# Kernel optimization log

Hardware: AMD Instinct MI355X
Metric: run time of the kernel (lower is better)

## Reference

```python
import jax, jax.numpy as jnp
import numpy as np

B, CIN, HALF, H, W = 4, 3, 32, 512, 512
K_MODE, PAD_MODE, N_LEVELS = 11, 5, 17  # 11x11 mode window, reflect pad 5, round(x*255/16) in 0..16
SLOPE, EPS = 0.01, 1e-5


def _leaky(x):
    return jnp.where(x > 0, x, SLOPE * x)


def _bn(x, g, b):
    # BatchNorm2d in training mode: batch statistics over (B,H,W), biased var
    m = x.mean(axis=(0, 2, 3), keepdims=True)
    v = x.var(axis=(0, 2, 3), keepdims=True)
    return (x - m) * jax.lax.rsqrt(v + EPS) * g[None, :, None, None] + b[None, :, None, None]


def _mode_pool(x):
    # quantize to 17 discrete levels, then sliding-window histogram mode (fused
    # equivalent of unfold + torch.mode; argmax first-hit == smallest tied value)
    k = jnp.clip(jnp.round(x * (255.0 / 16.0)), 0, N_LEVELS - 1).astype(jnp.int32)
    kp = jnp.pad(k, ((0, 0), (0, 0), (PAD_MODE, PAD_MODE), (PAD_MODE, PAD_MODE)), mode='reflect')
    onehot = (kp[..., None] == jnp.arange(N_LEVELS, dtype=jnp.int32)).astype(jnp.float32)
    counts = jax.lax.reduce_window(onehot, 0.0, jax.lax.add,
                                   (1, 1, K_MODE, K_MODE, 1), (1, 1, 1, 1, 1), 'VALID')
    mode_k = jnp.argmax(counts, axis=-1)  # [B,C,H,W]
    return mode_k.astype(jnp.float32) * (16.0 / 256.0)


def _nearest(x, Ho, Wo):
    # torch interpolate(mode='nearest'): src = floor(dst * in/out)
    hi, wi = x.shape[2], x.shape[3]
    ri = (jnp.arange(Ho) * hi) // Ho
    ci = (jnp.arange(Wo) * wi) // Wo
    return x[:, :, ri][:, :, :, ci]


def _forward(x, w1, b1, w2, b2, bn1_g, bn1_b, w3, b3, bn2_g, bn2_b,
             k_down, k_w, bnw_g, bnw_b, k_h, bnh_g, bnh_b):
    xm = _mode_pool(x)  # [B,CIN,H,W]
    # prepare: 1x1 conv -> LeakyReLU -> 1x1 conv -> BN -> LeakyReLU -> depthwise 1x1 -> BN -> LeakyReLU
    h = _leaky(jnp.einsum('bchw,oc->bohw', xm, w1) + b1[None, :, None, None])
    h = jnp.einsum('bchw,oc->bohw', h, w2) + b2[None, :, None, None]
    h = _leaky(_bn(h, bn1_g, bn1_b))
    h = h * w3[None, :, None, None] + b3[None, :, None, None]  # groups=half 1x1 conv
    h = _leaky(_bn(h, bn2_g, bn2_b))
    Bs, half, Ho, Wo = h.shape
    score = jnp.zeros((Bs, 2 * half, Ho, Wo), jnp.float32)
    d = h
    while min(d.shape[2], d.shape[3]) >= 3:  # static pyramid: 512->171->57->19->7->3->1
        d = jax.lax.conv_general_dilated(d, k_down, (3, 3), ((1, 1), (1, 1)),
                                         dimension_numbers=('NCHW', 'OIHW', 'NCHW'),
                                         feature_group_count=half)
        z = _nearest(d, Ho, Wo)
        wbr = _leaky(_bn(z * k_w[None, :, None, None], bnw_g, bnw_b))  # width branch (SharedConv k=1, no bias)
        hbr = _leaky(_bn(z * k_h[None, :, None, None], bnh_g, bnh_b))  # height branch
        # stack(dim=1).reshape => width channels first, then height channels
        score = score + jnp.concatenate([wbr, hbr], axis=1)
    return score


def setup_inputs():
    key = jax.random.key(0)
    ks = jax.random.split(key, 8)
    x = jax.random.uniform(ks[0], (B, CIN, H, W), dtype=jnp.float32)
    s1, s2 = 1.0 / np.sqrt(CIN), 1.0 / np.sqrt(2 * CIN)
    return {
        'x': x,
        'w1': jax.random.uniform(ks[1], (2 * CIN, CIN), jnp.float32, -s1, s1),
        'b1': jax.random.uniform(ks[2], (2 * CIN,), jnp.float32, -s1, s1),
        'w2': jax.random.uniform(ks[3], (HALF, 2 * CIN), jnp.float32, -s2, s2),
        'b2': jax.random.uniform(ks[4], (HALF,), jnp.float32, -s2, s2),
        'bn1_g': jnp.ones((HALF,), jnp.float32),
        'bn1_b': jnp.zeros((HALF,), jnp.float32),
        'w3': jax.random.uniform(ks[5], (HALF,), jnp.float32, -1.0, 1.0),
        'b3': jax.random.uniform(ks[6], (HALF,), jnp.float32, -1.0, 1.0),
        'bn2_g': jnp.ones((HALF,), jnp.float32),
        'bn2_b': jnp.zeros((HALF,), jnp.float32),
        'k_down': jnp.full((HALF, 1, 3, 3), 0.5, jnp.float32),  # SharedConv init
        'k_w': jnp.full((HALF,), 0.5, jnp.float32),
        'bnw_g': jnp.ones((HALF,), jnp.float32),
        'bnw_b': jnp.zeros((HALF,), jnp.float32),
        'k_h': jnp.full((HALF,), 0.5, jnp.float32),
        'bnh_g': jnp.ones((HALF,), jnp.float32),
        'bnh_b': jnp.zeros((HALF,), jnp.float32),
    }


def reference(x, w1, b1, w2, b2, bn1_g, bn1_b, w3, b3, bn2_g, bn2_b,
              k_down, k_w, bnw_g, bnw_b, k_h, bnh_g, bnh_b):
    return _forward(x, w1, b1, w2, b2, bn1_g, bn1_b, w3, b3, bn2_g, bn2_b,
                    k_down, k_w, bnw_g, bnw_b, k_h, bnh_g, bnh_b)
```

## Files before the change

### kernel.cpp

```cpp
#include <hip/hip_runtime.h>

#define HH 512
#define WW 512
#define HW 262144
#define NPIX 1048576
#define NPIXF 1048576.0f

typedef float f4 __attribute__((ext_vector_type(4)));

__device__ __forceinline__ float leaky(float v) { return v > 0.f ? v : 0.01f * v; }

__device__ __forceinline__ float repw(int i, int s) {
    return (float)(((i + 1) * 512 + s - 1) / s - (i * 512 + s - 1) / s);
}

__device__ __forceinline__ void hins(unsigned long long& h0, unsigned long long& h1,
                                     unsigned& c16, int val) {
    unsigned long long inc = 1ull << ((val & 7) * 8);
    h0 += (val < 8) ? inc : 0;
    h1 += (val >= 8 && val < 16) ? inc : 0;
    c16 += (unsigned)(val >> 4);
}
__device__ __forceinline__ void hrem(unsigned long long& h0, unsigned long long& h1,
                                     unsigned& c16, int val) {
    unsigned long long inc = 1ull << ((val & 7) * 8);
    h0 -= (val < 8) ? inc : 0;
    h1 -= (val >= 8 && val < 16) ? inc : 0;
    c16 -= (unsigned)(val >> 4);
}

__global__ __launch_bounds__(256) void mode_kernel(const float* __restrict__ x,
                                                   unsigned char* __restrict__ modeq) {
    __shared__ unsigned char q[26 * 272];
    __shared__ unsigned ch[2][267 * 5];
    const int plane = blockIdx.z;
    const int tc0 = blockIdx.x * 256;
    const int tr0 = blockIdx.y * 16;
    const float* xp = x + (size_t)plane * HW;
    for (int idx = threadIdx.x; idx < 26 * 266; idx += 256) {
        int r = idx / 266;
        int cc = idx - r * 266;
        int gr = tr0 + r - 5; gr = gr < 0 ? -gr : (gr > 511 ? 1022 - gr : gr);
        int gc = tc0 + cc - 5; gc = gc < 0 ? -gc : (gc > 511 ? 1022 - gc : gc);
        float v = rintf(xp[gr * WW + gc] * 15.9375f);
        v = fminf(fmaxf(v, 0.f), 16.f);
        q[r * 272 + cc] = (unsigned char)(int)v;
    }
    const int t = threadIdx.x;
    unsigned long long A0 = 0, A1 = 0; unsigned A2 = 0;
    unsigned long long B0 = 0, B1 = 0; unsigned B2 = 0;
    __syncthreads();
    for (int r = 0; r < 16; ++r) {
        if (r == 0) {
            #pragma unroll
            for (int v = 0; v < 11; ++v) {
                hins(A0, A1, A2, q[v * 272 + t]);
                if (t < 10) hins(B0, B1, B2, q[v * 272 + 256 + t]);
            }
        } else {
            hrem(A0, A1, A2, q[(r - 1) * 272 + t]);
            hins(A0, A1, A2, q[(r + 10) * 272 + t]);
            if (t < 10) {
                hrem(B0, B1, B2, q[(r - 1) * 272 + 256 + t]);
                hins(B0, B1, B2, q[(r + 10) * 272 + 256 + t]);
            }
        }
        unsigned* cb = ch[r & 1];
        cb[t * 5 + 0] = (unsigned)A0;
        cb[t * 5 + 1] = (unsigned)(A0 >> 32);
        cb[t * 5 + 2] = (unsigned)A1;
        cb[t * 5 + 3] = (unsigned)(A1 >> 32);
        cb[t * 5 + 4] = A2;
        if (t < 10) {
            cb[(256 + t) * 5 + 0] = (unsigned)B0;
            cb[(256 + t) * 5 + 1] = (unsigned)(B0 >> 32);
            cb[(256 + t) * 5 + 2] = (unsigned)B1;
            cb[(256 + t) * 5 + 3] = (unsigned)(B1 >> 32);
            cb[(256 + t) * 5 + 4] = B2;
        }
        __syncthreads();
        unsigned long long H0 = 0, H1 = 0; unsigned C = 0;
        #pragma unroll
        for (int v = 0; v < 11; ++v) {
            const unsigned* p = &cb[(t + v) * 5];
            H0 += (unsigned long long)p[0] | ((unsigned long long)p[1] << 32);
            H1 += (unsigned long long)p[2] | ((unsigned long long)p[3] << 32);
            C += p[4];
        }
        unsigned m = 0;
        #pragma unroll
        for (int i = 0; i < 8; ++i) {
            unsigned cnt = (unsigned)(H0 >> (8 * i)) & 0xFFu;
            unsigned val = (cnt << 8) | (unsigned)(16 - i);
            m = m > val ? m : val;
        }
        #pragma unroll
        for (int i = 8; i < 16; ++i) {
            unsigned cnt = (unsigned)(H1 >> (8 * (i - 8))) & 0xFFu;
            unsigned val = (cnt << 8) | (unsigned)(16 - i);
            m = m > val ? m : val;
        }
        unsigned val16 = (C << 8);
        m = m > val16 ? m : val16;
        int k = 16 - (int)(m & 0xFFu);
        modeq[(size_t)plane * HW + (size_t)(tr0 + r) * WW + tc0 + t] = (unsigned char)k;
    }
}

__global__ __launch_bounds__(256) void hist_kernel(const unsigned char* __restrict__ modeq,
                                                   const float* __restrict__ w1,
                                                   const float* __restrict__ b1,
                                                   unsigned* __restrict__ partial,
                                                   float* __restrict__ mpart) {
    __shared__ unsigned lh[4913];
    __shared__ float mred[27][4];
    for (int i = threadIdx.x; i < 4913; i += 256) lh[i] = 0;
    __syncthreads();
    int base = blockIdx.x * 8192;
    int b = base >> 18;
    int hw0 = base & (HW - 1);
    const unsigned char* mp = modeq + (size_t)b * 3 * HW;
    #pragma unroll
    for (int j = 0; j < 8; ++j) {
        int g = threadIdx.x + 256 * j;
        int hw = hw0 + g * 4;
        unsigned u0 = *(const unsigned*)(mp + hw);
        unsigned u1 = *(const unsigned*)(mp + hw + HW);
        unsigned u2 = *(const unsigned*)(mp + hw + 2 * HW);
        #pragma unroll
        for (int k = 0; k < 4; ++k) {
            int k0 = (u0 >> (8 * k)) & 0xFF;
            int k1 = (u1 >> (8 * k)) & 0xFF;
            int k2 = (u2 >> (8 * k)) & 0xFF;
            atomicAdd(&lh[k0 + 17 * k1 + 289 * k2], 1u);
        }
    }
    __syncthreads();
    unsigned* pp = partial + blockIdx.x * 4913;
    for (int i = threadIdx.x; i < 4913; i += 256) pp[i] = lh[i];
    float w1r[18], b1r[6];
    #pragma unroll
    for (int k = 0; k < 18; ++k) w1r[k] = w1[k];
    #pragma unroll
    for (int o = 0; o < 6; ++o) b1r[o] = b1[o];
    float M[27];
    #pragma unroll
    for (int i = 0; i < 27; ++i) M[i] = 0.f;
    for (int bin = threadIdx.x; bin < 4913; bin += 256) {
        float cnt = (float)lh[bin];
        int k0 = bin % 17;
        int r = bin / 17;
        int k1 = r % 17;
        int k2 = r / 17;
        float xm0 = k0 * 0.0625f, xm1 = k1 * 0.0625f, xm2 = k2 * 0.0625f;
        float t1[6];
        #pragma unroll
        for (int o = 0; o < 6; ++o)
            t1[o] = leaky(xm0 * w1r[o * 3] + xm1 * w1r[o * 3 + 1] + xm2 * w1r[o * 3 + 2] + b1r[o]);
        #pragma unroll
        for (int o = 0; o < 6; ++o) M[o] += cnt * t1[o];
        int ii = 6;
        #pragma unroll
        for (int j = 0; j < 6; ++j)
            #pragma unroll
            for (int k = j; k < 6; ++k) { M[ii] += cnt * t1[j] * t1[k]; ++ii; }
    }
    int wv = threadIdx.x >> 6;
    #pragma unroll
    for (int i = 0; i < 27; ++i) {
        float v = M[i];
        #pragma unroll
        for (int off = 32; off >= 1; off >>= 1) v += __shfl_xor(v, off);
        if ((threadIdx.x & 63) == 0) mred[i][wv] = v;
    }
    __syncthreads();
    if (threadIdx.x < 27)
        mpart[blockIdx.x * 27 + threadIdx.x] =
            mred[threadIdx.x][0] + mred[threadIdx.x][1] +
            mred[threadIdx.x][2] + mred[threadIdx.x][3];
}

__global__ __launch_bounds__(256) void redA_kernel(const unsigned* __restrict__ partial,
                                                   float* __restrict__ histf,
                                                   const float* __restrict__ mpart,
                                                   const float* __restrict__ w2,
                                                   const float* __restrict__ b2,
                                                   const float* __restrict__ g1,
                                                   const float* __restrict__ bb1,
                                                   float* __restrict__ p1) {
    if (blockIdx.x < 20) {
        int bin = blockIdx.x * 256 + threadIdx.x;
        if (bin >= 4913) return;
        unsigned s = 0;
        for (int blk = 0; blk < 128; ++blk) s += partial[blk * 4913 + bin];
        histf[bin] = (float)s;
        return;
    }
    __shared__ float mom[27];
    int t = threadIdx.x;
    if (t < 27) {
        float s = 0.f;
        for (int blk = 0; blk < 128; ++blk) s += mpart[blk * 27 + t];
        mom[t] = s;
    }
    __syncthreads();
    if (t < 32) {
        float w2r[6];
        #pragma unroll
        for (int k = 0; k < 6; ++k) w2r[k] = w2[t * 6 + k];
        float b2c = b2[t];
        float wm1 = 0.f;
        #pragma unroll
        for (int k = 0; k < 6; ++k) wm1 += w2r[k] * mom[k];
        float q = 0.f;
        int ii = 6;
        #pragma unroll
        for (int j = 0; j < 6; ++j)
            #pragma unroll
            for (int k = j; k < 6; ++k) {
                float f = w2r[j] * w2r[k] * mom[ii];
                q += (j == k) ? f : 2.f * f;
                ++ii;
            }
        float mean = b2c + wm1 / NPIXF;
        float ex2 = b2c * b2c + 2.f * b2c * (wm1 / NPIXF) + q / NPIXF;
        float var = ex2 - mean * mean;
        float a = g1[t] * rsqrtf(var + 1e-5f);
        p1[t] = a;
        p1[32 + t] = bb1[t] - mean * a;
    }
}

__global__ __launch_bounds__(256) void solveB2_kernel(const float* __restrict__ histf,
                                                      const float* __restrict__ w1,
                                                      const float* __restrict__ b1,
                                                      const float* __restrict__ w2,
                                                      const float* __restrict__ b2,
                                                      const float* __restrict__ p1,
                                                      const float* __restrict__ w3,
                                                      const float* __restrict__ b3,
                                                      const float* __restrict__ g,
                                                      const float* __restrict__ bb,
                                                      float* __restrict__ p2) {
    __shared__ float rs[4], rq[4];
    int c = blockIdx.x;
    float w1r[18], b1r[6], w2r[6];
    #pragma unroll
    for (int k = 0; k < 18; ++k) w1r[k] = w1[k];
    #pragma unroll
    for (int o = 0; o < 6; ++o) b1r[o] = b1[o];
    #pragma unroll
    for (int k = 0; k < 6; ++k) w2r[k] = w2[c * 6 + k];
    float b2c = b2[c];
    float a1 = p1[c], c1 = p1[32 + c];
    float sm = 0.f, sq = 0.f;
    for (int bin = threadIdx.x; bin < 4913; bin += 256) {
        float cnt = histf[bin];
        int k0 = bin % 17;
        int r = bin / 17;
        int k1 = r % 17;
        int k2 = r / 17;
        float xm0 = k0 * 0.0625f, xm1 = k1 * 0.0625f, xm2 = k2 * 0.0625f;
        float t1[6];
        #pragma unroll
        for (int o = 0; o < 6; ++o)
            t1[o] = leaky(xm0 * w1r[o * 3] + xm1 * w1r[o * 3 + 1] + xm2 * w1r[o * 3 + 2] + b1r[o]);
        float h2 = b2c;
        #pragma unroll
        for (int k = 0; k < 6; ++k) h2 += w2r[k] * t1[k];
        float tt = leaky(a1 * h2 + c1);
        sm += cnt * tt;
        sq += cnt * tt * tt;
    }
    #pragma unroll
    for (int off = 32; off >= 1; off >>= 1) {
        sm += __shfl_xor(sm, off);
        sq += __shfl_xor(sq, off);
    }
    if ((threadIdx.x & 63) == 0) { rs[threadIdx.x >> 6] = sm; rq[threadIdx.x >> 6] = sq; }
    __syncthreads();
    if (threadIdx.x == 0) {
        float s = rs[0] + rs[1] + rs[2] + rs[3];
        float qq = rq[0] + rq[1] + rq[2] + rq[3];
        float mt = s / NPIXF;
        float vt = qq / NPIXF - mt * mt;
        float m2 = w3[c] * mt + b3[c];
        float v2 = w3[c] * w3[c] * vt;
        float a = g[c] * rsqrtf(v2 + 1e-5f);
        p2[c] = a;
        p2[32 + c] = bb[c] - m2 * a;
    }
}

__global__ __launch_bounds__(64) void d1_kernel(const unsigned char* __restrict__ modeq,
                                                const float* __restrict__ w1,
                                                const float* __restrict__ b1,
                                                const float* __restrict__ w2,
                                                const float* __restrict__ b2,
                                                const float* __restrict__ w3,
                                                const float* __restrict__ b3,
                                                const float* __restrict__ p1,
                                                const float* __restrict__ p2,
                                                const float* __restrict__ kd,
                                                float* __restrict__ d1) {
    int j = blockIdx.x * 64 + threadIdx.x;
    if (j >= 171) return;
    int i = blockIdx.y;
    int b = blockIdx.z;
    float acc[32];
    #pragma unroll
    for (int c = 0; c < 32; ++c) acc[c] = 0.f;
    const unsigned char* mp = modeq + (size_t)b * 3 * HW;
    #pragma unroll
    for (int u = 0; u < 3; ++u) {
        int r = 3 * i - 1 + u;
        if (r < 0 || r > 511) continue;
        #pragma unroll
        for (int v = 0; v < 3; ++v) {
            int col = 3 * j - 1 + v;
            if (col < 0 || col > 511) continue;
            int off = r * WW + col;
            float xm0 = mp[off] * 0.0625f, xm1 = mp[off + HW] * 0.0625f, xm2 = mp[off + 2 * HW] * 0.0625f;
            float t1[6];
            #pragma unroll
            for (int o = 0; o < 6; ++o)
                t1[o] = leaky(xm0 * w1[o * 3] + xm1 * w1[o * 3 + 1] + xm2 * w1[o * 3 + 2] + b1[o]);
            #pragma unroll
            for (int c = 0; c < 32; ++c) {
                float h2 = b2[c];
                #pragma unroll
                for (int k = 0; k < 6; ++k) h2 += w2[c * 6 + k] * t1[k];
                float t = leaky(h2 * p1[c] + p1[32 + c]);
                float uu = t * w3[c] + b3[c];
                float hv = leaky(uu * p2[c] + p2[32 + c]);
                acc[c] += hv * kd[c * 9 + u * 3 + v];
            }
        }
    }
    size_t base = ((size_t)(b * 32) * 171 + i) * 171 + j;
    #pragma unroll
    for (int c = 0; c < 32; ++c) d1[base + (size_t)c * 29241] = acc[c];
}

__device__ __forceinline__ void red_store(float sm, float sq, float* rsc, float* ps) {
    #pragma unroll
    for (int off = 32; off >= 1; off >>= 1) {
        sm += __shfl_xor(sm, off);
        sq += __shfl_xor(sq, off);
    }
    __syncthreads();
    int wv = threadIdx.x >> 6;
    if ((threadIdx.x & 63) == 0) { rsc[wv] = sm; rsc[8 + wv] = sq; }
    __syncthreads();
    if (threadIdx.x == 0) {
        ps[0] = rsc[0] + rsc[1] + rsc[2] + rsc[3];
        ps[1] = rsc[8] + rsc[9] + rsc[10] + rsc[11];
    }
}

__device__ __forceinline__ void lvl(const float* src, int sin, float* dstL,
                                    float* dstG, int sout, const float* kreg,
                                    float* rsc, float* ps) {
    float sm = 0.f, sq = 0.f;
    int n = sout * sout;
    for (int i = threadIdx.x; i < n; i += 256) {
        int oi = i / sout, oj = i - oi * sout;
        float acc = 0.f;
        #pragma unroll
        for (int u = 0; u < 3; ++u) {
            int r = 3 * oi - 1 + u;
            if ((unsigned)r >= (unsigned)sin) continue;
            #pragma unroll
            for (int v = 0; v < 3; ++v) {
                int cc = 3 * oj - 1 + v;
                if ((unsigned)cc >= (unsigned)sin) continue;
                acc += src[r * sin + cc] * kreg[u * 3 + v];
            }
        }
        dstG[i] = acc;
        if (dstL) dstL[i] = acc;
        float w = repw(oi, sout) * repw(oj, sout);
        sm += w * acc;
        sq += w * acc * acc;
    }
    red_store(sm, sq, rsc, ps);
}

__global__ __launch_bounds__(256) void pyramid_kernel(const float* __restrict__ d1,
                                                      float* __restrict__ d2,
                                                      float* __restrict__ d3,
                                                      float* __restrict__ d4,
                                                      float* __restrict__ d5,
                                                      float* __restrict__ d6,
                                                      const float* __restrict__ kd,
                                                      float* __restrict__ pstats) {
    __shared__ float buf2[3249];
    __shared__ float buf3[361];
    __shared__ float buf4[49];
    __shared__ float buf5[9];
    __shared__ float rsc[16];
    int bc = blockIdx.x;
    int c = bc & 31;
    float kreg[9];
    #pragma unroll
    for (int qq = 0; qq < 9; ++qq) kreg[qq] = kd[c * 9 + qq];
    float* ps = pstats + (size_t)bc * 12;
    const float* s1 = d1 + (size_t)bc * 29241;
    float sm = 0.f, sq = 0.f;
    for (int i = threadIdx.x; i < 29241; i += 256) {
        int oi = i / 171, oj = i - oi * 171;
        float w = repw(oi, 171) * repw(oj, 171);
        float v = s1[i];
        sm += w * v;
        sq += w * v * v;
    }
    red_store(sm, sq, rsc, ps + 0);
    lvl(s1, 171, buf2, d2 + (size_t)bc * 3249, 57, kreg, rsc, ps + 2);
    lvl(buf2, 57, buf3, d3 + (size_t)bc * 361, 19, kreg, rsc, ps + 4);
    lvl(buf3, 19, buf4, d4 + (size_t)bc * 49, 7, kreg, rsc, ps + 6);
    lvl(buf4, 7, buf5, d5 + (size_t)bc * 9, 3, kreg, rsc, ps + 8);
    lvl(buf5, 3, nullptr, d6 + bc, 1, kreg, rsc, ps + 10);
}

__global__ void fin3_kernel(const float* __restrict__ pstats, const float* __restrict__ kw,
                            const float* __restrict__ gw, const float* __restrict__ bw,
                            const float* __restrict__ kh, const float* __restrict__ gh,
                            const float* __restrict__ bh, float* __restrict__ lp) {
    int t = threadIdx.x;
    if (t >= 192) return;
    int l = t >> 5, c = t & 31;
    float sm = 0.f, sq = 0.f;
    #pragma unroll
    for (int b = 0; b < 4; ++b) {
        const float* ps = pstats + (size_t)(b * 32 + c) * 12 + 2 * l;
        sm += ps[0];
        sq += ps[1];
    }
    float mz = sm / NPIXF;
    float vz = sq / NPIXF - mz * mz;
    float kwc = kw[c];
    float aw = gw[c] * rsqrtf(kwc * kwc * vz + 1e-5f);
    float khc = kh[c];
    float ah = gh[c] * rsqrtf(khc * khc * vz + 1e-5f);
    float* o = lp + (size_t)(l * 32 + c) * 4;
    o[0] = kwc * aw;
    o[1] = bw[c] - kwc * mz * aw;
    o[2] = khc * ah;
    o[3] = bh[c] - khc * mz * ah;
}

__global__ __launch_bounds__(256) void final_kernel(const float* __restrict__ d1,
                                                    const float* __restrict__ d2,
                                                    const float* __restrict__ d3,
                                                    const float* __restrict__ d4,
                                                    const float* __restrict__ d5,
                                                    const float* __restrict__ d6,
                                                    const float* __restrict__ lp,
                                                    float* __restrict__ out) {
    const float* ds[6] = {d1, d2, d3, d4, d5, d6};
    const int ss[6] = {171, 57, 19, 7, 3, 1};
    int idx = blockIdx.x * 256 + threadIdx.x;
    #pragma unroll 1
    for (int it = 0; it < 16; ++it, idx += 524288) {
        int w4 = (idx & 127) << 2;
        int h = (idx >> 7) & 511;
        int c = (idx >> 16) & 31;
        int b = idx >> 21;
        float accw[4] = {0.f, 0.f, 0.f, 0.f};
        float acch[4] = {0.f, 0.f, 0.f, 0.f};
        #pragma unroll
        for (int l = 0; l < 6; ++l) {
            int s = ss[l];
            int sh = (h * s) >> 9;
            const float* base = ds[l] + ((size_t)(b * 32 + c) * s + sh) * s;
            const float* a = lp + (size_t)(l * 32 + c) * 4;
            float a0 = a[0], a1 = a[1], a2 = a[2], a3 = a[3];
            #pragma unroll
            for (int k = 0; k < 4; ++k) {
                int sw = ((w4 + k) * s) >> 9;
                float val = base[sw];
                accw[k] += leaky(val * a0 + a1);
                acch[k] += leaky(val * a2 + a3);
            }
        }
        size_t o = (((size_t)(b * 64 + c)) << 18) + ((size_t)h << 9) + w4;
        f4 vw = {accw[0], accw[1], accw[2], accw[3]};
        f4 vh = {acch[0], acch[1], acch[2], acch[3]};
        __builtin_nontemporal_store(vw, (f4*)(out + o));
        __builtin_nontemporal_store(vh, (f4*)(out + o + (((size_t)32) << 18)));
    }
}

extern "C" void kernel_launch(void* const* d_in, const int* in_sizes, int n_in,
                              void* d_out, int out_size, void* d_ws, size_t ws_size,
                              hipStream_t stream) {
    const float* x     = (const float*)d_in[0];
    const float* w1    = (const float*)d_in[1];
    const float* b1    = (const float*)d_in[2];
    const float* w2    = (const float*)d_in[3];
    const float* b2    = (const float*)d_in[4];
    const float* bn1g  = (const float*)d_in[5];
    const float* bn1b  = (const float*)d_in[6];
    const float* w3    = (const float*)d_in[7];
    const float* b3    = (const float*)d_in[8];
    const float* bn2g  = (const float*)d_in[9];
    const float* bn2b  = (const float*)d_in[10];
    const float* kd    = (const float*)d_in[11];
    const float* kw    = (const float*)d_in[12];
    const float* bnwg  = (const float*)d_in[13];
    const float* bnwb  = (const float*)d_in[14];
    const float* kh    = (const float*)d_in[15];
    const float* bnhg  = (const float*)d_in[16];
    const float* bnhb  = (const float*)d_in[17];
    float* out = (float*)d_out;

    char* ws = (char*)d_ws;
    unsigned char* modeq = (unsigned char*)ws;
    float* mpart  = (float*)(ws + 3145728);
    float* tpart  = (float*)(ws + 3145728 + 13824);
    float* pstats = (float*)(ws + 3145728 + 13824 + 8192);
    float* p1 = (float*)(ws + 3174400);
    float* p2 = p1 + 64;
    float* lp = p2 + 64;
    float* histf = (float*)(ws + 3178496);
    unsigned* partial = (unsigned*)(ws + 3178496 + 20480);
    float* d1 = (float*)(ws + 3198976 + 2515456);
    float* d2 = d1 + 3742848;
    float* d3 = d2 + 415872;
    float* d4 = d3 + 46208;
    float* d5 = d4 + 6272;
    float* d6 = d5 + 1152;
    (void)tpart;

    mode_kernel<<<dim3(2, 32, 12), 256, 0, stream>>>(x, modeq);
    hist_kernel<<<128, 256, 0, stream>>>(modeq, w1, b1, partial, mpart);
    redA_kernel<<<21, 256, 0, stream>>>(partial, histf, mpart, w2, b2, bn1g, bn1b, p1);
    solveB2_kernel<<<32, 256, 0, stream>>>(histf, w1, b1, w2, b2, p1,
                                           w3, b3, bn2g, bn2b, p2);
    d1_kernel<<<dim3(3, 171, 4), 64, 0, stream>>>(modeq, w1, b1, w2, b2, w3, b3,
                                                  p1, p2, kd, d1);
    pyramid_kernel<<<128, 256, 0, stream>>>(d1, d2, d3, d4, d5, d6, kd, pstats);
    fin3_kernel<<<1, 192, 0, stream>>>(pstats, kw, bnwg, bnwb, kh, bnhg, bnhb, lp);
    final_kernel<<<2048, 256, 0, stream>>>(d1, d2, d3, d4, d5, d6, lp, out);
}
```

Baseline: 468.3 us.

## Drop shared column-histogram exchange in mode kernel; double hist kernel blocks

The mode kernel no longer keeps per-column histograms and combines 11 of them through shared memory with a barrier every output row. Each thread now holds a full 11x11 window histogram and slides it down by removing and adding whole 11-byte rows, read from shared memory as three 32-bit words. This removes the per-row syncthreads and the 5-word shared-memory traffic, but each thread does 22 histogram updates per row instead of 2. Separately, the histogram kernel launches 256 blocks over half as many pixels each, which doubles the partial buffers and the reduction loop length.

```diff
diff --git a/kernel.cpp b/kernel.cpp
--- a/kernel.cpp
+++ b/kernel.cpp
@@ -29,10 +29,48 @@
     c16 -= (unsigned)(val >> 4);
 }
 
+__device__ __forceinline__ void win3(const unsigned char* q, int rr, int t,
+                                     unsigned& w0, unsigned& w1, unsigned& w2) {
+    const unsigned* p = (const unsigned*)(q + rr * 272 + (t & ~3));
+    unsigned a0 = p[0], a1 = p[1], a2 = p[2], a3 = p[3];
+    int sh = (t & 3) * 8;
+    unsigned long long u01 = ((unsigned long long)a1 << 32) | a0;
+    unsigned long long u12 = ((unsigned long long)a2 << 32) | a1;
+    unsigned long long u23 = ((unsigned long long)a3 << 32) | a2;
+    w0 = (unsigned)(u01 >> sh);
+    w1 = (unsigned)(u12 >> sh);
+    w2 = (unsigned)(u23 >> sh);
+}
+
+__device__ __forceinline__ void winadd(const unsigned char* q, int rr, int t,
+                                       unsigned long long& H0, unsigned long long& H1,
+                                       unsigned& C) {
+    unsigned w0, w1, w2;
+    win3(q, rr, t, w0, w1, w2);
+    #pragma unroll
+    for (int i = 0; i < 4; ++i) hins(H0, H1, C, (w0 >> (8 * i)) & 0xFF);
+    #pragma unroll
+    for (int i = 0; i < 4; ++i) hins(H0, H1, C, (w1 >> (8 * i)) & 0xFF);
+    #pragma unroll
+    for (int i = 0; i < 3; ++i) hins(H0, H1, C, (w2 >> (8 * i)) & 0xFF);
+}
+
+__device__ __forceinline__ void winrem(const unsigned char* q, int rr, int t,
+                                       unsigned long long& H0, unsigned long long& H1,
+                                       unsigned& C) {
+    unsigned w0, w1, w2;
+    win3(q, rr, t, w0, w1, w2);
+    #pragma unroll
+    for (int i = 0; i < 4; ++i) hrem(H0, H1, C, (w0 >> (8 * i)) & 0xFF);
+    #pragma unroll
+    for (int i = 0; i < 4; ++i) hrem(H0, H1, C, (w1 >> (8 * i)) & 0xFF);
+    #pragma unroll
+    for (int i = 0; i < 3; ++i) hrem(H0, H1, C, (w2 >> (8 * i)) & 0xFF);
+}
+
 __global__ __launch_bounds__(256) void mode_kernel(const float* __restrict__ x,
                                                    unsigned char* __restrict__ modeq) {
     __shared__ unsigned char q[26 * 272];
-    __shared__ unsigned ch[2][267 * 5];
     const int plane = blockIdx.z;
     const int tc0 = blockIdx.x * 256;
     const int tr0 = blockIdx.y * 16;
@@ -46,46 +84,16 @@
         v = fminf(fmaxf(v, 0.f), 16.f);
         q[r * 272 + cc] = (unsigned char)(int)v;
     }
+    __syncthreads();
     const int t = threadIdx.x;
-    unsigned long long A0 = 0, A1 = 0; unsigned A2 = 0;
-    unsigned long long B0 = 0, B1 = 0; unsigned B2 = 0;
-    __syncthreads();
+    unsigned long long H0 = 0, H1 = 0; unsigned C = 0;
+    #pragma unroll 1
+    for (int rr = 0; rr < 11; ++rr) winadd(q, rr, t, H0, H1, C);
+    #pragma unroll 1
     for (int r = 0; r < 16; ++r) {
-        if (r == 0) {
-            #pragma unroll
-            for (int v = 0; v < 11; ++v) {
-                hins(A0, A1, A2, q[v * 272 + t]);
-                if (t < 10) hins(B0, B1, B2, q[v * 272 + 256 + t]);
-            }
-        } else {
-            hrem(A0, A1, A2, q[(r - 1) * 272 + t]);
-            hins(A0, A1, A2, q[(r + 10) * 272 + t]);
-            if (t < 10) {
-                hrem(B0, B1, B2, q[(r - 1) * 272 + 256 + t]);
-                hins(B0, B1, B2, q[(r + 10) * 272 + 256 + t]);
-            }
-        }
-        unsigned* cb = ch[r & 1];
-        cb[t * 5 + 0] = (unsigned)A0;
-        cb[t * 5 + 1] = (unsigned)(A0 >> 32);
-        cb[t * 5 + 2] = (unsigned)A1;
-        cb[t * 5 + 3] = (unsigned)(A1 >> 32);
-        cb[t * 5 + 4] = A2;
-        if (t < 10) {
-            cb[(256 + t) * 5 + 0] = (unsigned)B0;
-            cb[(256 + t) * 5 + 1] = (unsigned)(B0 >> 32);
-            cb[(256 + t) * 5 + 2] = (unsigned)B1;
-            cb[(256 + t) * 5 + 3] = (unsigned)(B1 >> 32);
-            cb[(256 + t) * 5 + 4] = B2;
-        }
-        __syncthreads();
-        unsigned long long H0 = 0, H1 = 0; unsigned C = 0;
-        #pragma unroll
-        for (int v = 0; v < 11; ++v) {
-            const unsigned* p = &cb[(t + v) * 5];
-            H0 += (unsigned long long)p[0] | ((unsigned long long)p[1] << 32);
-            H1 += (unsigned long long)p[2] | ((unsigned long long)p[3] << 32);
-            C += p[4];
+        if (r > 0) {
+            winrem(q, r - 1, t, H0, H1, C);
+            winadd(q, r + 10, t, H0, H1, C);
         }
         unsigned m = 0;
         #pragma unroll
@@ -116,12 +124,12 @@
     __shared__ float mred[27][4];
     for (int i = threadIdx.x; i < 4913; i += 256) lh[i] = 0;
     __syncthreads();
-    int base = blockIdx.x * 8192;
+    int base = blockIdx.x * 4096;
     int b = base >> 18;
     int hw0 = base & (HW - 1);
     const unsigned char* mp = modeq + (size_t)b * 3 * HW;
     #pragma unroll
-    for (int j = 0; j < 8; ++j) {
+    for (int j = 0; j < 4; ++j) {
         int g = threadIdx.x + 256 * j;
         int hw = hw0 + g * 4;
         unsigned u0 = *(const unsigned*)(mp + hw);
@@ -192,7 +200,7 @@
         int bin = blockIdx.x * 256 + threadIdx.x;
         if (bin >= 4913) return;
         unsigned s = 0;
-        for (int blk = 0; blk < 128; ++blk) s += partial[blk * 4913 + bin];
+        for (int blk = 0; blk < 256; ++blk) s += partial[blk * 4913 + bin];
         histf[bin] = (float)s;
         return;
     }
@@ -200,7 +208,7 @@
     int t = threadIdx.x;
     if (t < 27) {
         float s = 0.f;
-        for (int blk = 0; blk < 128; ++blk) s += mpart[blk * 27 + t];
+        for (int blk = 0; blk < 256; ++blk) s += mpart[blk * 27 + t];
         mom[t] = s;
     }
     __syncthreads();
@@ -517,23 +525,21 @@
     char* ws = (char*)d_ws;
     unsigned char* modeq = (unsigned char*)ws;
     float* mpart  = (float*)(ws + 3145728);
-    float* tpart  = (float*)(ws + 3145728 + 13824);
-    float* pstats = (float*)(ws + 3145728 + 13824 + 8192);
-    float* p1 = (float*)(ws + 3174400);
+    float* pstats = (float*)(ws + 3145728 + 27648);
+    float* p1 = (float*)(ws + 3179520);
     float* p2 = p1 + 64;
     float* lp = p2 + 64;
-    float* histf = (float*)(ws + 3178496);
-    unsigned* partial = (unsigned*)(ws + 3178496 + 20480);
-    float* d1 = (float*)(ws + 3198976 + 2515456);
+    float* histf = (float*)(ws + 3183104);
+    unsigned* partial = (unsigned*)(ws + 3183104 + 19968);
+    float* d1 = (float*)(ws + 3203072 + 5030912);
     float* d2 = d1 + 3742848;
     float* d3 = d2 + 415872;
     float* d4 = d3 + 46208;
     float* d5 = d4 + 6272;
     float* d6 = d5 + 1152;
-    (void)tpart;
 
     mode_kernel<<<dim3(2, 32, 12), 256, 0, stream>>>(x, modeq);
-    hist_kernel<<<128, 256, 0, stream>>>(modeq, w1, b1, partial, mpart);
+    hist_kernel<<<256, 256, 0, stream>>>(modeq, w1, b1, partial, mpart);
     redA_kernel<<<21, 256, 0, stream>>>(partial, histf, mpart, w2, b2, bn1g, bn1b, p1);
     solveB2_kernel<<<32, 256, 0, stream>>>(histf, w1, b1, w2, b2, p1,
                                            w3, b3, bn2g, bn2b, p2);
```

After: 488.6 us. 4.3% more time.
